# Kernel tuning notes

Measured on AMD Instinct MI355X. Metric: run time of the kernel, lower is better.

The kernel has to match this reference:

```python
import jax, jax.numpy as jnp
import numpy as np

B, BOND, N, ATOM, UNITS = 256, 5, 128, 64, 128


def setup_inputs() -> dict:
    key = jax.random.key(0)
    k1, k2, k3 = jax.random.split(key, 3)
    adjacency = jax.random.uniform(k1, (B, BOND, N, N), dtype=jnp.float32)
    features = jax.random.normal(k2, (B, N, ATOM), dtype=jnp.float32)
    # per-sample unique kernel: (global_batch, bond_dim, atom_dim, units)
    kernel = jax.random.normal(k3, (B, BOND, ATOM, UNITS), dtype=jnp.float32) * 0.05
    return {"adjacency": adjacency, "features": features, "kernel": kernel}


def reference(adjacency, features, kernel):
    # aggregate neighbors per bond type: [B, bond, N, atom]
    x = jnp.einsum('bemn,bnd->bemd', adjacency, features)
    # per-sample, per-bond linear transform: [B, bond, N, units]
    x = jnp.einsum('bemd,bedu->bemu', x, kernel)
    # reduce over bond types, then activation: [B, N, units]
    return jax.nn.relu(jnp.sum(x, axis=1))
```

## Files before the change

### kernel.cpp

```cpp
#include <hip/hip_runtime.h>


typedef __attribute__((ext_vector_type(8))) short s8v;
typedef __attribute__((ext_vector_type(4))) float f4v;

__device__ __forceinline__ short f2bf(float f) {
    unsigned u = __builtin_bit_cast(unsigned, f);
    u += 0x7FFFu + ((u >> 16) & 1u);
    return (short)(u >> 16);
}

__device__ __forceinline__ void lds_barrier() {
    asm volatile("s_waitcnt lgkmcnt(0)" ::: "memory");
    __builtin_amdgcn_s_barrier();
    __builtin_amdgcn_sched_barrier(0);
}

__global__ __launch_bounds__(1024, 4)
void rgc_kernel(const float* __restrict__ adj,
                const float* __restrict__ feat,
                const float* __restrict__ ker,
                float* __restrict__ out)
{
    __shared__ __align__(16) short featB[16 * 512];
    __shared__ __align__(16) short kerB[2][16 * 512];
    __shared__ __align__(16) short YA[16][2 * 512];

    const int tid  = threadIdx.x;
    const int w    = tid >> 6;
    const int lane = tid & 63;
    const int c16  = lane & 15;
    const int quad = lane >> 4;
    const int g    = w >> 1;
    const int h    = w & 1;

    const int b = blockIdx.x;
    const float* adjB = adj  + (size_t)b * (5 * 128 * 128);
    const float* feG  = feat + (size_t)b * (128 * 64);
    const float* keG  = ker  + (size_t)b * (5 * 64 * 128);
    float*       outB = out  + (size_t)b * (128 * 128);

    f4v a0[4], a1[4];
    {
        const float* ap = adjB + (16 * g + c16) * 128 + 8 * quad;
        #pragma unroll
        for (int k16 = 0; k16 < 4; ++k16) {
            a0[k16] = *(const f4v*)(ap + 32 * k16);
            a1[k16] = *(const f4v*)(ap + 32 * k16 + 4);
        }
    }

    {
        const int fd  = tid & 63;
        const int fn0 = (tid >> 6) * 8;
        float fv[8];
        #pragma unroll
        for (int j = 0; j < 8; ++j)
            fv[j] = feG[(fn0 + j) * 64 + fd];
        s8v v;
        #pragma unroll
        for (int j = 0; j < 8; ++j) v[j] = f2bf(fv[j]);
        *(s8v*)&featB[((fd >> 4) * 4 + (fn0 >> 5)) * 512 + ((fn0 >> 3) & 3) * 128 + (fd & 15) * 8] = v;
    }

    const int ku  = tid & 127;
    const int kd0 = (tid >> 7) * 8;
    const int kerB_off = (ku >> 4) * 1024 + (kd0 >> 5) * 512 + ((kd0 >> 3) & 3) * 128 + (ku & 15) * 8;
    {
        float kv[8];
        #pragma unroll
        for (int j = 0; j < 8; ++j)
            kv[j] = keG[(kd0 + j) * 128 + ku];
        s8v v;
        #pragma unroll
        for (int j = 0; j < 8; ++j) v[j] = f2bf(kv[j]);
        *(s8v*)&kerB[0][kerB_off] = v;
    }
    lds_barrier();

    f4v oacc[4] = {};

    for (int e = 0; e < 5; ++e) {
        s8v af[4];
        #pragma unroll
        for (int k16 = 0; k16 < 4; ++k16) {
            #pragma unroll
            for (int j = 0; j < 4; ++j) {
                af[k16][j]     = f2bf(a0[k16][j]);
                af[k16][4 + j] = f2bf(a1[k16][j]);
            }
        }

        float kv[8];
        if (e < 4) {
            const float* kp = keG + (e + 1) * (64 * 128);
            #pragma unroll
            for (int j = 0; j < 8; ++j)
                kv[j] = kp[(kd0 + j) * 128 + ku];
            const float* ap = adjB + (e + 1) * (128 * 128) + (16 * g + c16) * 128 + 8 * quad;
            #pragma unroll
            for (int k16 = 0; k16 < 4; ++k16) {
                a0[k16] = *(const f4v*)(ap + 32 * k16);
                a1[k16] = *(const f4v*)(ap + 32 * k16 + 4);
            }
            __builtin_amdgcn_sched_barrier(0);
        }

        f4v yacc[4] = {};
        #pragma unroll
        for (int k16 = 0; k16 < 4; ++k16)
            #pragma unroll
            for (int d16 = 0; d16 < 4; ++d16) {
                s8v bf = *(const s8v*)&featB[(d16 * 4 + k16) * 512 + lane * 8];
                yacc[d16] = __builtin_amdgcn_mfma_f32_16x16x32_bf16(af[k16], bf, yacc[d16], 0, 0, 0);
            }

        #pragma unroll
        for (int d16 = 0; d16 < 4; ++d16) {
            const int base = (d16 >> 1) * 512 + ((2 * d16 + (c16 >> 3)) & 3) * 128 + (c16 & 7);
            #pragma unroll
            for (int r = 0; r < 4; ++r)
                YA[w][base + (4 * quad + r) * 8] = f2bf(yacc[d16][r]);
        }

        {
            const int buf = e & 1;
            s8v afr0 = *(const s8v*)&YA[w][lane * 8];
            s8v afr1 = *(const s8v*)&YA[w][512 + lane * 8];
            #pragma unroll
            for (int n = 0; n < 4; ++n) {
                const int u16 = 4 * h + n;
                s8v b0 = *(const s8v*)&kerB[buf][(u16 * 2 + 0) * 512 + lane * 8];
                s8v b1 = *(const s8v*)&kerB[buf][(u16 * 2 + 1) * 512 + lane * 8];
                oacc[n] = __builtin_amdgcn_mfma_f32_16x16x32_bf16(afr0, b0, oacc[n], 0, 0, 0);
                oacc[n] = __builtin_amdgcn_mfma_f32_16x16x32_bf16(afr1, b1, oacc[n], 0, 0, 0);
            }
        }

        if (e < 4) {
            s8v v;
            #pragma unroll
            for (int j = 0; j < 8; ++j) v[j] = f2bf(kv[j]);
            *(s8v*)&kerB[(e + 1) & 1][kerB_off] = v;
            lds_barrier();
        }
    }

    #pragma unroll
    for (int n = 0; n < 4; ++n)
        #pragma unroll
        for (int r = 0; r < 4; ++r)
            outB[(16 * g + 4 * quad + r) * 128 + 16 * (4 * h + n) + c16] = fmaxf(oacc[n][r], 0.f);
}

extern "C" void kernel_launch(void* const* d_in, const int* in_sizes, int n_in,
                              void* d_out, int out_size, void* d_ws, size_t ws_size,
                              hipStream_t stream)
{
    const float* adj  = (const float*)d_in[0];
    const float* feat = (const float*)d_in[1];
    const float* ker  = (const float*)d_in[2];
    rgc_kernel<<<256, 1024, 0, stream>>>(adj, feat, ker, (float*)d_out);
}
```

Baseline: 169.0 us.

## Split each sample across two 512-thread blocks by row halves with XCD-aware mapping

Each batch sample is now handled by two workgroups of 512 threads, each computing 64 of the 128 output rows, instead of one 1024-thread block. The block index is remapped so that the two halves of a sample and neighbouring samples land on the same XCD, which should improve L2 sharing of features and kernel weights. This doubles the grid to 512 blocks for better CU coverage and lowers per-block LDS use. In exchange, features and per-sample kernels are loaded and converted twice, once per half, and each thread now loads twice as much kernel data per bond step.

```diff
diff --git a/kernel.cpp b/kernel.cpp
--- a/kernel.cpp
+++ b/kernel.cpp
@@ -16,7 +16,7 @@
     __builtin_amdgcn_sched_barrier(0);
 }
 
-__global__ __launch_bounds__(1024, 4)
+__global__ __launch_bounds__(512, 4)
 void rgc_kernel(const float* __restrict__ adj,
                 const float* __restrict__ feat,
                 const float* __restrict__ ker,
@@ -24,7 +24,7 @@
 {
     __shared__ __align__(16) short featB[16 * 512];
     __shared__ __align__(16) short kerB[2][16 * 512];
-    __shared__ __align__(16) short YA[16][2 * 512];
+    __shared__ __align__(16) short YA[8][2 * 512];
 
     const int tid  = threadIdx.x;
     const int w    = tid >> 6;
@@ -34,7 +34,12 @@
     const int g    = w >> 1;
     const int h    = w & 1;
 
-    const int b = blockIdx.x;
+    const int bid  = blockIdx.x;
+    const int wg   = ((bid & 7) << 6) | (bid >> 3);
+    const int b    = wg >> 1;
+    const int half = wg & 1;
+    const int rowBase = 64 * half + 16 * g;
+
     const float* adjB = adj  + (size_t)b * (5 * 128 * 128);
     const float* feG  = feat + (size_t)b * (128 * 64);
     const float* keG  = ker  + (size_t)b * (5 * 64 * 128);
@@ -42,7 +47,7 @@
 
     f4v a0[4], a1[4];
     {
-        const float* ap = adjB + (16 * g + c16) * 128 + 8 * quad;
+        const float* ap = adjB + (rowBase + c16) * 128 + 8 * quad;
         #pragma unroll
         for (int k16 = 0; k16 < 4; ++k16) {
             a0[k16] = *(const f4v*)(ap + 32 * k16);
@@ -51,30 +56,37 @@
     }
 
     {
-        const int fd  = tid & 63;
-        const int fn0 = (tid >> 6) * 8;
-        float fv[8];
+        const int fd = tid & 63;
         #pragma unroll
-        for (int j = 0; j < 8; ++j)
-            fv[j] = feG[(fn0 + j) * 64 + fd];
-        s8v v;
-        #pragma unroll
-        for (int j = 0; j < 8; ++j) v[j] = f2bf(fv[j]);
-        *(s8v*)&featB[((fd >> 4) * 4 + (fn0 >> 5)) * 512 + ((fn0 >> 3) & 3) * 128 + (fd & 15) * 8] = v;
+        for (int i = 0; i < 2; ++i) {
+            const int fn0 = i * 64 + (tid >> 6) * 8;
+            float fv[8];
+            #pragma unroll
+            for (int j = 0; j < 8; ++j)
+                fv[j] = feG[(fn0 + j) * 64 + fd];
+            s8v v;
+            #pragma unroll
+            for (int j = 0; j < 8; ++j) v[j] = f2bf(fv[j]);
+            *(s8v*)&featB[((fd >> 4) * 4 + (fn0 >> 5)) * 512 + ((fn0 >> 3) & 3) * 128 + (fd & 15) * 8] = v;
+        }
     }
 
-    const int ku  = tid & 127;
-    const int kd0 = (tid >> 7) * 8;
-    const int kerB_off = (ku >> 4) * 1024 + (kd0 >> 5) * 512 + ((kd0 >> 3) & 3) * 128 + (ku & 15) * 8;
+    const int ku   = tid & 127;
+    const int kd0a = (tid >> 7) * 8;
+    const int kd0b = 32 + kd0a;
+    const int kOffA = (ku >> 4) * 1024 + (kd0a >> 5) * 512 + ((kd0a >> 3) & 3) * 128 + (ku & 15) * 8;
+    const int kOffB = (ku >> 4) * 1024 + (kd0b >> 5) * 512 + ((kd0b >> 3) & 3) * 128 + (ku & 15) * 8;
     {
-        float kv[8];
+        float kv[16];
         #pragma unroll
-        for (int j = 0; j < 8; ++j)
-            kv[j] = keG[(kd0 + j) * 128 + ku];
-        s8v v;
+        for (int j = 0; j < 8; ++j) kv[j]     = keG[(kd0a + j) * 128 + ku];
         #pragma unroll
-        for (int j = 0; j < 8; ++j) v[j] = f2bf(kv[j]);
-        *(s8v*)&kerB[0][kerB_off] = v;
+        for (int j = 0; j < 8; ++j) kv[8 + j] = keG[(kd0b + j) * 128 + ku];
+        s8v va, vb;
+        #pragma unroll
+        for (int j = 0; j < 8; ++j) { va[j] = f2bf(kv[j]); vb[j] = f2bf(kv[8 + j]); }
+        *(s8v*)&kerB[0][kOffA] = va;
+        *(s8v*)&kerB[0][kOffB] = vb;
     }
     lds_barrier();
 
@@ -91,13 +103,14 @@
             }
         }
 
-        float kv[8];
+        float kv[16];
         if (e < 4) {
             const float* kp = keG + (e + 1) * (64 * 128);
             #pragma unroll
-            for (int j = 0; j < 8; ++j)
-                kv[j] = kp[(kd0 + j) * 128 + ku];
-            const float* ap = adjB + (e + 1) * (128 * 128) + (16 * g + c16) * 128 + 8 * quad;
+            for (int j = 0; j < 8; ++j) kv[j]     = kp[(kd0a + j) * 128 + ku];
+            #pragma unroll
+            for (int j = 0; j < 8; ++j) kv[8 + j] = kp[(kd0b + j) * 128 + ku];
+            const float* ap = adjB + (e + 1) * (128 * 128) + (rowBase + c16) * 128 + 8 * quad;
             #pragma unroll
             for (int k16 = 0; k16 < 4; ++k16) {
                 a0[k16] = *(const f4v*)(ap + 32 * k16);
@@ -138,10 +151,11 @@
         }
 
         if (e < 4) {
-            s8v v;
+            s8v va, vb;
             #pragma unroll
-            for (int j = 0; j < 8; ++j) v[j] = f2bf(kv[j]);
-            *(s8v*)&kerB[(e + 1) & 1][kerB_off] = v;
+            for (int j = 0; j < 8; ++j) { va[j] = f2bf(kv[j]); vb[j] = f2bf(kv[8 + j]); }
+            *(s8v*)&kerB[(e + 1) & 1][kOffA] = va;
+            *(s8v*)&kerB[(e + 1) & 1][kOffB] = vb;
             lds_barrier();
         }
     }
@@ -150,7 +164,7 @@
     for (int n = 0; n < 4; ++n)
         #pragma unroll
         for (int r = 0; r < 4; ++r)
-            outB[(16 * g + 4 * quad + r) * 128 + 16 * (4 * h + n) + c16] = fmaxf(oacc[n][r], 0.f);
+            outB[(rowBase + 4 * quad + r) * 128 + 16 * (4 * h + n) + c16] = fmaxf(oacc[n][r], 0.f);
 }
 
 extern "C" void kernel_launch(void* const* d_in, const int* in_sizes, int n_in,
@@ -160,5 +174,5 @@
     const float* adj  = (const float*)d_in[0];
     const float* feat = (const float*)d_in[1];
     const float* ker  = (const float*)d_in[2];
-    rgc_kernel<<<256, 1024, 0, stream>>>(adj, feat, ker, (float*)d_out);
+    rgc_kernel<<<512, 512, 0, stream>>>(adj, feat, ker, (float*)d_out);
 }
```

Measured after the change: 178.3 us. +5.5%, slower.

## Stage adjacency through double-buffered LDS with contiguous coalesced global loads

Applied to the files above, without the earlier changes.

Adjacency is now loaded with each thread reading 16 contiguous floats. It is converted to bf16 and written into a double-buffered LDS tile in MFMA fragment layout, so MFMA operands are read back from LDS. The previous version had each lane gather strided 32-byte pieces directly into registers. The change targets better global coalescing and fewer registers, at the cost of about 64KB more LDS per block, which lowers occupancy and adds LDS traffic.

```diff
diff --git a/kernel.cpp b/kernel.cpp
--- a/kernel.cpp
+++ b/kernel.cpp
@@ -22,9 +22,10 @@
                 const float* __restrict__ ker,
                 float* __restrict__ out)
 {
+    __shared__ __align__(16) short adjF[2][32 * 512];
+    __shared__ __align__(16) short kerF[2][16 * 512];
     __shared__ __align__(16) short featB[16 * 512];
-    __shared__ __align__(16) short kerB[2][16 * 512];
-    __shared__ __align__(16) short YA[16][2 * 512];
+    __shared__ __align__(16) short YA[16][1024];
 
     const int tid  = threadIdx.x;
     const int w    = tid >> 6;
@@ -40,80 +41,77 @@
     const float* keG  = ker  + (size_t)b * (5 * 64 * 128);
     float*       outB = out  + (size_t)b * (128 * 128);
 
-    f4v a0[4], a1[4];
-    {
-        const float* ap = adjB + (16 * g + c16) * 128 + 8 * quad;
-        #pragma unroll
-        for (int k16 = 0; k16 < 4; ++k16) {
-            a0[k16] = *(const f4v*)(ap + 32 * k16);
-            a1[k16] = *(const f4v*)(ap + 32 * k16 + 4);
-        }
-    }
+    const int ar   = tid >> 3;
+    const int ap_  = tid & 7;
+    const int aOff = ((ar >> 4) * 4 + (ap_ >> 1)) * 512 + (16 * (2 * (ap_ & 1)) + (ar & 15)) * 8;
+    const float* aSrc = adjB + 16 * tid;
+
+    f4v ax[4];
+    #pragma unroll
+    for (int i = 0; i < 4; ++i) ax[i] = *(const f4v*)(aSrc + 4 * i);
+
+    const int fd  = tid & 63;
+    const int fn0 = (tid >> 6) * 8;
+    float fv[8];
+    #pragma unroll
+    for (int j = 0; j < 8; ++j) fv[j] = feG[(fn0 + j) * 64 + fd];
+
+    const int ku  = tid & 127;
+    const int kd0 = (tid >> 7) * 8;
+    const int kOff = (ku >> 4) * 1024 + (kd0 >> 5) * 512 + ((kd0 >> 3) & 3) * 128 + (ku & 15) * 8;
+    float kv[8];
+    #pragma unroll
+    for (int j = 0; j < 8; ++j) kv[j] = keG[(kd0 + j) * 128 + ku];
 
     {
-        const int fd  = tid & 63;
-        const int fn0 = (tid >> 6) * 8;
-        float fv[8];
+        s8v lo, hi;
         #pragma unroll
-        for (int j = 0; j < 8; ++j)
-            fv[j] = feG[(fn0 + j) * 64 + fd];
+        for (int j = 0; j < 4; ++j) {
+            lo[j] = f2bf(ax[0][j]); lo[4 + j] = f2bf(ax[1][j]);
+            hi[j] = f2bf(ax[2][j]); hi[4 + j] = f2bf(ax[3][j]);
+        }
+        *(s8v*)&adjF[0][aOff]       = lo;
+        *(s8v*)&adjF[0][aOff + 128] = hi;
+    }
+    {
         s8v v;
         #pragma unroll
         for (int j = 0; j < 8; ++j) v[j] = f2bf(fv[j]);
         *(s8v*)&featB[((fd >> 4) * 4 + (fn0 >> 5)) * 512 + ((fn0 >> 3) & 3) * 128 + (fd & 15) * 8] = v;
     }
-
-    const int ku  = tid & 127;
-    const int kd0 = (tid >> 7) * 8;
-    const int kerB_off = (ku >> 4) * 1024 + (kd0 >> 5) * 512 + ((kd0 >> 3) & 3) * 128 + (ku & 15) * 8;
     {
-        float kv[8];
-        #pragma unroll
-        for (int j = 0; j < 8; ++j)
-            kv[j] = keG[(kd0 + j) * 128 + ku];
         s8v v;
         #pragma unroll
         for (int j = 0; j < 8; ++j) v[j] = f2bf(kv[j]);
-        *(s8v*)&kerB[0][kerB_off] = v;
+        *(s8v*)&kerF[0][kOff] = v;
     }
     lds_barrier();
 
     f4v oacc[4] = {};
 
     for (int e = 0; e < 5; ++e) {
-        s8v af[4];
-        #pragma unroll
-        for (int k16 = 0; k16 < 4; ++k16) {
+        f4v ax2[4];
+        float kv2[8];
+        if (e < 4) {
+            const float* as = aSrc + (e + 1) * 16384;
             #pragma unroll
-            for (int j = 0; j < 4; ++j) {
-                af[k16][j]     = f2bf(a0[k16][j]);
-                af[k16][4 + j] = f2bf(a1[k16][j]);
-            }
-        }
-
-        float kv[8];
-        if (e < 4) {
+            for (int i = 0; i < 4; ++i) ax2[i] = *(const f4v*)(as + 4 * i);
             const float* kp = keG + (e + 1) * (64 * 128);
             #pragma unroll
-            for (int j = 0; j < 8; ++j)
-                kv[j] = kp[(kd0 + j) * 128 + ku];
-            const float* ap = adjB + (e + 1) * (128 * 128) + (16 * g + c16) * 128 + 8 * quad;
-            #pragma unroll
-            for (int k16 = 0; k16 < 4; ++k16) {
-                a0[k16] = *(const f4v*)(ap + 32 * k16);
-                a1[k16] = *(const f4v*)(ap + 32 * k16 + 4);
-            }
+            for (int j = 0; j < 8; ++j) kv2[j] = kp[(kd0 + j) * 128 + ku];
             __builtin_amdgcn_sched_barrier(0);
         }
 
         f4v yacc[4] = {};
         #pragma unroll
-        for (int k16 = 0; k16 < 4; ++k16)
+        for (int k16 = 0; k16 < 4; ++k16) {
+            s8v af = *(const s8v*)&adjF[e & 1][(g * 4 + k16) * 512 + lane * 8];
             #pragma unroll
             for (int d16 = 0; d16 < 4; ++d16) {
                 s8v bf = *(const s8v*)&featB[(d16 * 4 + k16) * 512 + lane * 8];
-                yacc[d16] = __builtin_amdgcn_mfma_f32_16x16x32_bf16(af[k16], bf, yacc[d16], 0, 0, 0);
+                yacc[d16] = __builtin_amdgcn_mfma_f32_16x16x32_bf16(af, bf, yacc[d16], 0, 0, 0);
             }
+        }
 
         #pragma unroll
         for (int d16 = 0; d16 < 4; ++d16) {
@@ -124,24 +122,31 @@
         }
 
         {
-            const int buf = e & 1;
             s8v afr0 = *(const s8v*)&YA[w][lane * 8];
             s8v afr1 = *(const s8v*)&YA[w][512 + lane * 8];
             #pragma unroll
             for (int n = 0; n < 4; ++n) {
                 const int u16 = 4 * h + n;
-                s8v b0 = *(const s8v*)&kerB[buf][(u16 * 2 + 0) * 512 + lane * 8];
-                s8v b1 = *(const s8v*)&kerB[buf][(u16 * 2 + 1) * 512 + lane * 8];
+                s8v b0 = *(const s8v*)&kerF[e & 1][(u16 * 2 + 0) * 512 + lane * 8];
+                s8v b1 = *(const s8v*)&kerF[e & 1][(u16 * 2 + 1) * 512 + lane * 8];
                 oacc[n] = __builtin_amdgcn_mfma_f32_16x16x32_bf16(afr0, b0, oacc[n], 0, 0, 0);
                 oacc[n] = __builtin_amdgcn_mfma_f32_16x16x32_bf16(afr1, b1, oacc[n], 0, 0, 0);
             }
         }
 
         if (e < 4) {
+            s8v lo, hi;
+            #pragma unroll
+            for (int j = 0; j < 4; ++j) {
+                lo[j] = f2bf(ax2[0][j]); lo[4 + j] = f2bf(ax2[1][j]);
+                hi[j] = f2bf(ax2[2][j]); hi[4 + j] = f2bf(ax2[3][j]);
+            }
+            *(s8v*)&adjF[(e + 1) & 1][aOff]       = lo;
+            *(s8v*)&adjF[(e + 1) & 1][aOff + 128] = hi;
             s8v v;
             #pragma unroll
-            for (int j = 0; j < 8; ++j) v[j] = f2bf(kv[j]);
-            *(s8v*)&kerB[(e + 1) & 1][kerB_off] = v;
+            for (int j = 0; j < 8; ++j) v[j] = f2bf(kv2[j]);
+            *(s8v*)&kerF[(e + 1) & 1][kOff] = v;
             lds_barrier();
         }
     }
```

New measurement: 169.3 us. Within noise of the previous version (+0.2%).
